# Kernel optimization log

Measured on AMD Instinct MI355X. Metric: run time of the kernel, lower is better.

The kernel has to match this reference:

```python
import jax, jax.numpy as jnp
import numpy as np

TEMPERATURE = 0.5
EPS = 1e-12  # matches torch F.normalize default eps


def _l2_normalize(x):
    norm = jnp.sqrt(jnp.sum(x * x, axis=-1, keepdims=True))
    return x / jnp.maximum(norm, EPS)


def setup_inputs() -> dict:
    key = jax.random.key(0)
    k1, k2 = jax.random.split(key)
    B, C, D = 64, 512, 256
    visual_features = jax.random.normal(k1, (B, C, D), dtype=jnp.float32)
    text_embeddings = jax.random.normal(k2, (B, C, D), dtype=jnp.float32)
    return {"visual_features": visual_features, "text_embeddings": text_embeddings}


def reference(visual_features, text_embeddings):
    v = _l2_normalize(visual_features)   # (B, C, D)
    t = _l2_normalize(text_embeddings)   # (B, C, D)
    # positive: diagonal similarity per class
    sim_pos = jnp.einsum('bcd,bcd->bc', v, t)
    positive = jnp.exp(sim_pos / TEMPERATURE)            # (B, C)
    # full BxCxC similarity matrix
    all_sim = jnp.exp(jnp.einsum('bcd,bkd->bck', v, t) / TEMPERATURE)
    negative = jnp.sum(all_sim, axis=-1) - positive      # (B, C)
    loss = -jnp.log(positive / (positive + negative))
    return jnp.mean(loss)
```

## Files before the change

### kernel.cpp

```cpp
#include <hip/hip_runtime.h>
#include <hip/hip_bf16.h>

#define BB 64
#define CC 512
#define DD 256

typedef __attribute__((ext_vector_type(8))) short bf16x8;
typedef __attribute__((ext_vector_type(4))) float f32x4;

__device__ inline short f2bf(float f) {
    union { __hip_bfloat16 h; short s; } cv;
    cv.h = __float2bfloat16(f);
    return cv.s;
}

__global__ __launch_bounds__(256, 1) void gemm_loss(const float* __restrict__ V,
                                                    const float* __restrict__ T,
                                                    float* __restrict__ partials) {
    extern __shared__ char lds[];
    char* As  = lds;
    char* Bs0 = lds + 65536;
    char* Bs1 = lds + 65536 + 32768;

    const int i0 = blockIdx.x;
    const int b  = (i0 & 7) * 8 + (i0 >> 5);
    const int rb = (i0 >> 3) & 3;

    const int tid  = threadIdx.x;
    const int lane = tid & 63;
    const int wave = tid >> 6;
    const int wr = wave >> 1;
    const int wc = wave & 1;
    const int g  = lane >> 4;
    const int ln = lane & 15;

    const float* gV = V + (size_t)b * (CC * DD) + (size_t)rb * 128 * DD;
    const float* gT = T + (size_t)b * (CC * DD);

    const int rrow = tid >> 3;
    const int ecol = (tid & 7) * 32;

    {
        float4 ar[4][8];
#pragma unroll
        for (int p = 0; p < 4; ++p) {
            const float4* src =
                reinterpret_cast<const float4*>(gV + (size_t)(p * 32 + rrow) * DD + ecol);
#pragma unroll
            for (int q = 0; q < 8; ++q) ar[p][q] = src[q];
        }
#pragma unroll
        for (int p = 0; p < 4; ++p) {
            float ss = 0.f;
#pragma unroll
            for (int q = 0; q < 8; ++q)
                ss += ar[p][q].x * ar[p][q].x + ar[p][q].y * ar[p][q].y +
                      ar[p][q].z * ar[p][q].z + ar[p][q].w * ar[p][q].w;
            ss += __shfl_xor(ss, 1);
            ss += __shfl_xor(ss, 2);
            ss += __shfl_xor(ss, 4);
            const float rinv = 1.0f / fmaxf(sqrtf(ss), 1e-12f);
            const int row = p * 32 + rrow;
            char* dstrow  = As + row * 512;
            const int sw  = (row & 7) << 4;
#pragma unroll
            for (int q2 = 0; q2 < 4; ++q2) {
                const float4 v0 = ar[p][2 * q2], v1 = ar[p][2 * q2 + 1];
                bf16x8 o;
                o[0] = f2bf(v0.x * rinv); o[1] = f2bf(v0.y * rinv);
                o[2] = f2bf(v0.z * rinv); o[3] = f2bf(v0.w * rinv);
                o[4] = f2bf(v1.x * rinv); o[5] = f2bf(v1.y * rinv);
                o[6] = f2bf(v1.z * rinv); o[7] = f2bf(v1.w * rinv);
                const int bc = ecol * 2 + q2 * 16;
                *reinterpret_cast<bf16x8*>(dstrow + (bc ^ sw)) = o;
            }
        }
    }
    {
#pragma unroll
        for (int p = 0; p < 2; ++p) {
            const float4* src =
                reinterpret_cast<const float4*>(gT + (size_t)(p * 32 + rrow) * DD + ecol);
            float4 x[8];
#pragma unroll
            for (int q = 0; q < 8; ++q) x[q] = src[q];
            float ss = 0.f;
#pragma unroll
            for (int q = 0; q < 8; ++q)
                ss += x[q].x * x[q].x + x[q].y * x[q].y + x[q].z * x[q].z + x[q].w * x[q].w;
            ss += __shfl_xor(ss, 1);
            ss += __shfl_xor(ss, 2);
            ss += __shfl_xor(ss, 4);
            const float rinv = 1.0f / fmaxf(sqrtf(ss), 1e-12f);
            const int row = p * 32 + rrow;
            char* dstrow  = Bs0 + row * 512;
            const int sw  = (row & 7) << 4;
#pragma unroll
            for (int q2 = 0; q2 < 4; ++q2) {
                const float4 v0 = x[2 * q2], v1 = x[2 * q2 + 1];
                bf16x8 o;
                o[0] = f2bf(v0.x * rinv); o[1] = f2bf(v0.y * rinv);
                o[2] = f2bf(v0.z * rinv); o[3] = f2bf(v0.w * rinv);
                o[4] = f2bf(v1.x * rinv); o[5] = f2bf(v1.y * rinv);
                o[6] = f2bf(v1.z * rinv); o[7] = f2bf(v1.w * rinv);
                const int bc = ecol * 2 + q2 * 16;
                *reinterpret_cast<bf16x8*>(dstrow + (bc ^ sw)) = o;
            }
        }
    }
    __syncthreads();

    bf16x8 a[4][8];
#pragma unroll
    for (int i = 0; i < 4; ++i) {
        const int row  = wr * 64 + i * 16 + ln;
        const char* rp = As + row * 512;
        const int sw   = (row & 7) << 4;
#pragma unroll
        for (int kk = 0; kk < 8; ++kk)
            a[i][kk] = *reinterpret_cast<const bf16x8*>(rp + ((kk * 64 + g * 16) ^ sw));
    }

    float rs[4][4];
    float dg[4][4];
#pragma unroll
    for (int i = 0; i < 4; ++i)
#pragma unroll
        for (int r = 0; r < 4; ++r) { rs[i][r] = 0.f; dg[i][r] = 0.f; }

    const f32x4 fzero = {0.f, 0.f, 0.f, 0.f};
    float4 br[2][8];
    int cur = 0;

    for (int ct = 0; ct < 8; ++ct) {
        if (ct < 7) {
            const float* gB = gT + (size_t)(ct + 1) * 64 * DD;
#pragma unroll
            for (int p = 0; p < 2; ++p) {
                const float4* src =
                    reinterpret_cast<const float4*>(gB + (size_t)(p * 32 + rrow) * DD + ecol);
#pragma unroll
                for (int q = 0; q < 8; ++q) br[p][q] = src[q];
            }
        }

        char* Bc = cur ? Bs1 : Bs0;
        f32x4 acc[4][2];
#pragma unroll
        for (int i = 0; i < 4; ++i)
#pragma unroll
            for (int j = 0; j < 2; ++j) acc[i][j] = fzero;

#pragma unroll
        for (int kk = 0; kk < 8; ++kk) {
            bf16x8 bb[2];
#pragma unroll
            for (int j = 0; j < 2; ++j) {
                const int row = wc * 32 + j * 16 + ln;
                bb[j] = *reinterpret_cast<const bf16x8*>(
                    Bc + row * 512 + (((kk * 64 + g * 16)) ^ ((row & 7) << 4)));
            }
#pragma unroll
            for (int i = 0; i < 4; ++i)
#pragma unroll
                for (int j = 0; j < 2; ++j)
                    acc[i][j] =
                        __builtin_amdgcn_mfma_f32_16x16x32_bf16(a[i][kk], bb[j], acc[i][j], 0, 0, 0);
        }

        const int gcb = ct * 64 + wc * 32;
#pragma unroll
        for (int i = 0; i < 4; ++i) {
            const int grow = rb * 128 + wr * 64 + i * 16 + g * 4;
#pragma unroll
            for (int j = 0; j < 2; ++j) {
                const int gcol = gcb + j * 16 + ln;
#pragma unroll
                for (int r = 0; r < 4; ++r) {
                    const float s2 = acc[i][j][r] * 2.0f;
                    rs[i][r] += __expf(s2);
                    if (gcol == grow + r) dg[i][r] += s2;
                }
            }
        }

        if (ct < 7) {
            char* Bn = cur ? Bs0 : Bs1;
#pragma unroll
            for (int p = 0; p < 2; ++p) {
                float ss = 0.f;
#pragma unroll
                for (int q = 0; q < 8; ++q)
                    ss += br[p][q].x * br[p][q].x + br[p][q].y * br[p][q].y +
                          br[p][q].z * br[p][q].z + br[p][q].w * br[p][q].w;
                ss += __shfl_xor(ss, 1);
                ss += __shfl_xor(ss, 2);
                ss += __shfl_xor(ss, 4);
                const float rinv = 1.0f / fmaxf(sqrtf(ss), 1e-12f);
                const int row = p * 32 + rrow;
                char* dstrow  = Bn + row * 512;
                const int sw  = (row & 7) << 4;
#pragma unroll
                for (int q2 = 0; q2 < 4; ++q2) {
                    const float4 v0 = br[p][2 * q2], v1 = br[p][2 * q2 + 1];
                    bf16x8 o;
                    o[0] = f2bf(v0.x * rinv); o[1] = f2bf(v0.y * rinv);
                    o[2] = f2bf(v0.z * rinv); o[3] = f2bf(v0.w * rinv);
                    o[4] = f2bf(v1.x * rinv); o[5] = f2bf(v1.y * rinv);
                    o[6] = f2bf(v1.z * rinv); o[7] = f2bf(v1.w * rinv);
                    const int bc = ecol * 2 + q2 * 16;
                    *reinterpret_cast<bf16x8*>(dstrow + (bc ^ sw)) = o;
                }
            }
        }
        __syncthreads();
        cur ^= 1;
    }

    float* vred = reinterpret_cast<float*>(lds);
    float* dred = vred + 256;
    float* red  = vred + 512;
#pragma unroll
    for (int i = 0; i < 4; ++i)
#pragma unroll
        for (int r = 0; r < 4; ++r) {
            float v = rs[i][r];
            float d = dg[i][r];
#pragma unroll
            for (int m = 1; m < 16; m <<= 1) {
                v += __shfl_xor(v, m);
                d += __shfl_xor(d, m);
            }
            if (ln == 0) {
                const int rl = wr * 64 + i * 16 + g * 4 + r;
                vred[rl * 2 + wc] = v;
                dred[rl * 2 + wc] = d;
            }
        }
    __syncthreads();

    float lsum = 0.f;
    if (tid < 128) {
        const float vv = vred[tid * 2] + vred[tid * 2 + 1];
        const float dd = dred[tid * 2] + dred[tid * 2 + 1];
        lsum = logf(vv) - dd;
    }
#pragma unroll
    for (int m = 1; m < 64; m <<= 1) lsum += __shfl_xor(lsum, m);
    if (lane == 0) red[wave] = lsum;
    __syncthreads();
    if (tid == 0) partials[blockIdx.x] = red[0] + red[1] + red[2] + red[3];
}

__global__ __launch_bounds__(256) void final_reduce(const float* __restrict__ partials,
                                                    float* __restrict__ out) {
    const int t = threadIdx.x;
    float v = partials[t];
#pragma unroll
    for (int m = 1; m < 64; m <<= 1) v += __shfl_xor(v, m);
    __shared__ float red[4];
    if ((t & 63) == 0) red[t >> 6] = v;
    __syncthreads();
    if (t == 0) out[0] = (red[0] + red[1] + red[2] + red[3]) * (1.0f / 32768.0f);
}

extern "C" void kernel_launch(void* const* d_in, const int* in_sizes, int n_in,
                              void* d_out, int out_size, void* d_ws, size_t ws_size,
                              hipStream_t stream) {
    const float* vis = (const float*)d_in[0];
    const float* txt = (const float*)d_in[1];

    float* partials = (float*)d_ws;
    float* out      = (float*)d_out;

    hipFuncSetAttribute((const void*)gemm_loss, hipFuncAttributeMaxDynamicSharedMemorySize,
                        131072);

    gemm_loss<<<256, 256, 131072, stream>>>(vis, txt, partials);
    final_reduce<<<1, 256, 0, stream>>>(partials, out);
}
```

Measured before the change: 43.95 us.

## Halve row tile to 64, launch 512 blocks with two-buffer LDS reuse

Each block now handles 64 visual rows instead of 128, so the grid doubles to 512 blocks and LDS per block drops from 128KB to 64KB, which allows two blocks per CU. The A tile is read into registers and its LDS buffer is then reused as the second B ping-pong buffer. Waves now split the column tile, one 16-column strip each, rather than a 2x2 arrangement. The aim is better occupancy and a more even spread of work across the CUs. The cost is that each text tile is loaded and normalized twice as often in total.

```diff
diff --git a/kernel.cpp b/kernel.cpp
--- a/kernel.cpp
+++ b/kernel.cpp
@@ -7,6 +7,8 @@
 
 typedef __attribute__((ext_vector_type(8))) short bf16x8;
 typedef __attribute__((ext_vector_type(4))) float f32x4;
+
+#define SW(row) (((row) & 7) << 4)
 
 __device__ inline short f2bf(float f) {
     union { __hip_bfloat16 h; short s; } cv;
@@ -14,112 +16,85 @@
     return cv.s;
 }
 
-__global__ __launch_bounds__(256, 1) void gemm_loss(const float* __restrict__ V,
+__device__ inline void reduce_write(char* dst_base, int row, int ecolB, const float4* x) {
+    float ss = 0.f;
+#pragma unroll
+    for (int q = 0; q < 8; ++q)
+        ss += x[q].x * x[q].x + x[q].y * x[q].y + x[q].z * x[q].z + x[q].w * x[q].w;
+    ss += __shfl_xor(ss, 1);
+    ss += __shfl_xor(ss, 2);
+    ss += __shfl_xor(ss, 4);
+    const float rinv = 1.0f / fmaxf(sqrtf(ss), 1e-12f);
+    char* dstrow = dst_base + row * 512;
+    const int sw = SW(row);
+#pragma unroll
+    for (int q2 = 0; q2 < 4; ++q2) {
+        const float4 v0 = x[2 * q2], v1 = x[2 * q2 + 1];
+        bf16x8 o;
+        o[0] = f2bf(v0.x * rinv); o[1] = f2bf(v0.y * rinv);
+        o[2] = f2bf(v0.z * rinv); o[3] = f2bf(v0.w * rinv);
+        o[4] = f2bf(v1.x * rinv); o[5] = f2bf(v1.y * rinv);
+        o[6] = f2bf(v1.z * rinv); o[7] = f2bf(v1.w * rinv);
+        *reinterpret_cast<bf16x8*>(dstrow + ((ecolB + q2 * 16) ^ sw)) = o;
+    }
+}
+
+__global__ __launch_bounds__(256, 2) void gemm_loss(const float* __restrict__ V,
                                                     const float* __restrict__ T,
                                                     float* __restrict__ partials) {
     extern __shared__ char lds[];
-    char* As  = lds;
-    char* Bs0 = lds + 65536;
-    char* Bs1 = lds + 65536 + 32768;
+    char* BufA = lds;
+    char* BufB = lds + 32768;
 
     const int i0 = blockIdx.x;
-    const int b  = (i0 & 7) * 8 + (i0 >> 5);
-    const int rb = (i0 >> 3) & 3;
+    const int b  = (i0 & 7) * 8 + ((i0 >> 3) & 7);
+    const int rb = i0 >> 6;
 
     const int tid  = threadIdx.x;
     const int lane = tid & 63;
     const int wave = tid >> 6;
-    const int wr = wave >> 1;
-    const int wc = wave & 1;
-    const int g  = lane >> 4;
-    const int ln = lane & 15;
-
-    const float* gV = V + (size_t)b * (CC * DD) + (size_t)rb * 128 * DD;
+    const int g    = lane >> 4;
+    const int ln   = lane & 15;
+    const int rrow = tid >> 3;
+    const int ecolB = (tid & 7) * 64;
+
+    const float* gV = V + (size_t)b * (CC * DD) + (size_t)rb * 64 * DD;
     const float* gT = T + (size_t)b * (CC * DD);
 
-    const int rrow = tid >> 3;
-    const int ecol = (tid & 7) * 32;
-
     {
-        float4 ar[4][8];
-#pragma unroll
-        for (int p = 0; p < 4; ++p) {
-            const float4* src =
-                reinterpret_cast<const float4*>(gV + (size_t)(p * 32 + rrow) * DD + ecol);
-#pragma unroll
-            for (int q = 0; q < 8; ++q) ar[p][q] = src[q];
-        }
-#pragma unroll
-        for (int p = 0; p < 4; ++p) {
-            float ss = 0.f;
-#pragma unroll
-            for (int q = 0; q < 8; ++q)
-                ss += ar[p][q].x * ar[p][q].x + ar[p][q].y * ar[p][q].y +
-                      ar[p][q].z * ar[p][q].z + ar[p][q].w * ar[p][q].w;
-            ss += __shfl_xor(ss, 1);
-            ss += __shfl_xor(ss, 2);
-            ss += __shfl_xor(ss, 4);
-            const float rinv = 1.0f / fmaxf(sqrtf(ss), 1e-12f);
-            const int row = p * 32 + rrow;
-            char* dstrow  = As + row * 512;
-            const int sw  = (row & 7) << 4;
-#pragma unroll
-            for (int q2 = 0; q2 < 4; ++q2) {
-                const float4 v0 = ar[p][2 * q2], v1 = ar[p][2 * q2 + 1];
-                bf16x8 o;
-                o[0] = f2bf(v0.x * rinv); o[1] = f2bf(v0.y * rinv);
-                o[2] = f2bf(v0.z * rinv); o[3] = f2bf(v0.w * rinv);
-                o[4] = f2bf(v1.x * rinv); o[5] = f2bf(v1.y * rinv);
-                o[6] = f2bf(v1.z * rinv); o[7] = f2bf(v1.w * rinv);
-                const int bc = ecol * 2 + q2 * 16;
-                *reinterpret_cast<bf16x8*>(dstrow + (bc ^ sw)) = o;
-            }
-        }
-    }
-    {
+        float4 xs[4][8];
 #pragma unroll
         for (int p = 0; p < 2; ++p) {
             const float4* src =
-                reinterpret_cast<const float4*>(gT + (size_t)(p * 32 + rrow) * DD + ecol);
-            float4 x[8];
-#pragma unroll
-            for (int q = 0; q < 8; ++q) x[q] = src[q];
-            float ss = 0.f;
-#pragma unroll
-            for (int q = 0; q < 8; ++q)
-                ss += x[q].x * x[q].x + x[q].y * x[q].y + x[q].z * x[q].z + x[q].w * x[q].w;
-            ss += __shfl_xor(ss, 1);
-            ss += __shfl_xor(ss, 2);
-            ss += __shfl_xor(ss, 4);
-            const float rinv = 1.0f / fmaxf(sqrtf(ss), 1e-12f);
-            const int row = p * 32 + rrow;
-            char* dstrow  = Bs0 + row * 512;
-            const int sw  = (row & 7) << 4;
-#pragma unroll
-            for (int q2 = 0; q2 < 4; ++q2) {
-                const float4 v0 = x[2 * q2], v1 = x[2 * q2 + 1];
-                bf16x8 o;
-                o[0] = f2bf(v0.x * rinv); o[1] = f2bf(v0.y * rinv);
-                o[2] = f2bf(v0.z * rinv); o[3] = f2bf(v0.w * rinv);
-                o[4] = f2bf(v1.x * rinv); o[5] = f2bf(v1.y * rinv);
-                o[6] = f2bf(v1.z * rinv); o[7] = f2bf(v1.w * rinv);
-                const int bc = ecol * 2 + q2 * 16;
-                *reinterpret_cast<bf16x8*>(dstrow + (bc ^ sw)) = o;
-            }
-        }
+                reinterpret_cast<const float4*>(gV + (size_t)(p * 32 + rrow) * DD + (tid & 7) * 32);
+#pragma unroll
+            for (int q = 0; q < 8; ++q) xs[p][q] = src[q];
+        }
+#pragma unroll
+        for (int p = 0; p < 2; ++p) {
+            const float4* src =
+                reinterpret_cast<const float4*>(gT + (size_t)(p * 32 + rrow) * DD + (tid & 7) * 32);
+#pragma unroll
+            for (int q = 0; q < 8; ++q) xs[2 + p][q] = src[q];
+        }
+#pragma unroll
+        for (int p = 0; p < 2; ++p) reduce_write(BufA, p * 32 + rrow, ecolB, xs[p]);
+#pragma unroll
+        for (int p = 0; p < 2; ++p) reduce_write(BufB, p * 32 + rrow, ecolB, xs[2 + p]);
     }
     __syncthreads();
 
     bf16x8 a[4][8];
 #pragma unroll
     for (int i = 0; i < 4; ++i) {
-        const int row  = wr * 64 + i * 16 + ln;
-        const char* rp = As + row * 512;
-        const int sw   = (row & 7) << 4;
+        const int row  = i * 16 + ln;
+        const char* rp = BufA + row * 512;
+        const int sw   = SW(row);
 #pragma unroll
         for (int kk = 0; kk < 8; ++kk)
             a[i][kk] = *reinterpret_cast<const bf16x8*>(rp + ((kk * 64 + g * 16) ^ sw));
     }
+    __syncthreads();
 
     float rs[4][4];
     float dg[4][4];
@@ -128,98 +103,61 @@
 #pragma unroll
         for (int r = 0; r < 4; ++r) { rs[i][r] = 0.f; dg[i][r] = 0.f; }
 
-    const f32x4 fzero = {0.f, 0.f, 0.f, 0.f};
-    float4 br[2][8];
-    int cur = 0;
+    float4 x[8];
 
     for (int ct = 0; ct < 8; ++ct) {
         if (ct < 7) {
-            const float* gB = gT + (size_t)(ct + 1) * 64 * DD;
-#pragma unroll
-            for (int p = 0; p < 2; ++p) {
-                const float4* src =
-                    reinterpret_cast<const float4*>(gB + (size_t)(p * 32 + rrow) * DD + ecol);
-#pragma unroll
-                for (int q = 0; q < 8; ++q) br[p][q] = src[q];
-            }
-        }
-
-        char* Bc = cur ? Bs1 : Bs0;
-        f32x4 acc[4][2];
-#pragma unroll
-        for (int i = 0; i < 4; ++i)
-#pragma unroll
-            for (int j = 0; j < 2; ++j) acc[i][j] = fzero;
-
-#pragma unroll
-        for (int kk = 0; kk < 8; ++kk) {
-            bf16x8 bb[2];
-#pragma unroll
-            for (int j = 0; j < 2; ++j) {
-                const int row = wc * 32 + j * 16 + ln;
-                bb[j] = *reinterpret_cast<const bf16x8*>(
-                    Bc + row * 512 + (((kk * 64 + g * 16)) ^ ((row & 7) << 4)));
-            }
-#pragma unroll
-            for (int i = 0; i < 4; ++i)
-#pragma unroll
-                for (int j = 0; j < 2; ++j)
-                    acc[i][j] =
-                        __builtin_amdgcn_mfma_f32_16x16x32_bf16(a[i][kk], bb[j], acc[i][j], 0, 0, 0);
-        }
-
-        const int gcb = ct * 64 + wc * 32;
+            const float4* src = reinterpret_cast<const float4*>(
+                gT + (size_t)((ct + 1) * 64 + rrow) * DD + (tid & 7) * 32);
+#pragma unroll
+            for (int q = 0; q < 8; ++q) x[q] = src[q];
+        }
+
+        const char* Bc = (ct & 1) ? BufA : BufB;
+        f32x4 acc[4];
+#pragma unroll
+        for (int i = 0; i < 4; ++i) acc[i] = (f32x4){0.f, 0.f, 0.f, 0.f};
+        {
+            const int row  = wave * 16 + ln;
+            const char* rp = Bc + row * 512;
+            const int sw   = SW(row);
+#pragma unroll
+            for (int kk = 0; kk < 8; ++kk) {
+                const bf16x8 bb =
+                    *reinterpret_cast<const bf16x8*>(rp + ((kk * 64 + g * 16) ^ sw));
+#pragma unroll
+                for (int i = 0; i < 4; ++i)
+                    acc[i] = __builtin_amdgcn_mfma_f32_16x16x32_bf16(a[i][kk], bb, acc[i], 0, 0, 0);
+            }
+        }
+
+        char* Bn = (ct & 1) ? BufB : BufA;
+        if (ct < 7) {
+            reduce_write(Bn, rrow, ecolB, x);
+            const float4* src = reinterpret_cast<const float4*>(
+                gT + (size_t)((ct + 1) * 64 + 32 + rrow) * DD + (tid & 7) * 32);
+#pragma unroll
+            for (int q = 0; q < 8; ++q) x[q] = src[q];
+        }
+
+        const int gcol = ct * 64 + wave * 16 + ln;
 #pragma unroll
         for (int i = 0; i < 4; ++i) {
-            const int grow = rb * 128 + wr * 64 + i * 16 + g * 4;
-#pragma unroll
-            for (int j = 0; j < 2; ++j) {
-                const int gcol = gcb + j * 16 + ln;
-#pragma unroll
-                for (int r = 0; r < 4; ++r) {
-                    const float s2 = acc[i][j][r] * 2.0f;
-                    rs[i][r] += __expf(s2);
-                    if (gcol == grow + r) dg[i][r] += s2;
-                }
-            }
-        }
-
-        if (ct < 7) {
-            char* Bn = cur ? Bs0 : Bs1;
-#pragma unroll
-            for (int p = 0; p < 2; ++p) {
-                float ss = 0.f;
-#pragma unroll
-                for (int q = 0; q < 8; ++q)
-                    ss += br[p][q].x * br[p][q].x + br[p][q].y * br[p][q].y +
-                          br[p][q].z * br[p][q].z + br[p][q].w * br[p][q].w;
-                ss += __shfl_xor(ss, 1);
-                ss += __shfl_xor(ss, 2);
-                ss += __shfl_xor(ss, 4);
-                const float rinv = 1.0f / fmaxf(sqrtf(ss), 1e-12f);
-                const int row = p * 32 + rrow;
-                char* dstrow  = Bn + row * 512;
-                const int sw  = (row & 7) << 4;
-#pragma unroll
-                for (int q2 = 0; q2 < 4; ++q2) {
-                    const float4 v0 = br[p][2 * q2], v1 = br[p][2 * q2 + 1];
-                    bf16x8 o;
-                    o[0] = f2bf(v0.x * rinv); o[1] = f2bf(v0.y * rinv);
-                    o[2] = f2bf(v0.z * rinv); o[3] = f2bf(v0.w * rinv);
-                    o[4] = f2bf(v1.x * rinv); o[5] = f2bf(v1.y * rinv);
-                    o[6] = f2bf(v1.z * rinv); o[7] = f2bf(v1.w * rinv);
-                    const int bc = ecol * 2 + q2 * 16;
-                    *reinterpret_cast<bf16x8*>(dstrow + (bc ^ sw)) = o;
-                }
-            }
-        }
+            const int grow = rb * 64 + i * 16 + g * 4;
+#pragma unroll
+            for (int r = 0; r < 4; ++r) {
+                const float s2 = acc[i][r] * 2.0f;
+                rs[i][r] += __expf(s2);
+                if (gcol == grow + r) dg[i][r] += s2;
+            }
+        }
+
+        if (ct < 7) reduce_write(Bn, 32 + rrow, ecolB, x);
         __syncthreads();
-        cur ^= 1;
-    }
-
-    float* vred = reinterpret_cast<float*>(lds);
+    }
+
+    float* vred = reinterpret_cast<float*>(BufB);
     float* dred = vred + 256;
-    float* red  = vred + 512;
 #pragma unroll
     for (int i = 0; i < 4; ++i)
 #pragma unroll
@@ -232,30 +170,27 @@
                 d += __shfl_xor(d, m);
             }
             if (ln == 0) {
-                const int rl = wr * 64 + i * 16 + g * 4 + r;
-                vred[rl * 2 + wc] = v;
-                dred[rl * 2 + wc] = d;
-            }
-        }
-    __syncthreads();
-
-    float lsum = 0.f;
-    if (tid < 128) {
-        const float vv = vred[tid * 2] + vred[tid * 2 + 1];
-        const float dd = dred[tid * 2] + dred[tid * 2 + 1];
-        lsum = logf(vv) - dd;
-    }
-#pragma unroll
-    for (int m = 1; m < 64; m <<= 1) lsum += __shfl_xor(lsum, m);
-    if (lane == 0) red[wave] = lsum;
-    __syncthreads();
-    if (tid == 0) partials[blockIdx.x] = red[0] + red[1] + red[2] + red[3];
+                const int rl = i * 16 + g * 4 + r;
+                vred[rl * 4 + wave] = v;
+                dred[rl * 4 + wave] = d;
+            }
+        }
+    __syncthreads();
+
+    if (wave == 0) {
+        const float vv = vred[lane * 4] + vred[lane * 4 + 1] + vred[lane * 4 + 2] + vred[lane * 4 + 3];
+        const float dd = dred[lane * 4] + dred[lane * 4 + 1] + dred[lane * 4 + 2] + dred[lane * 4 + 3];
+        float lsum = logf(vv) - dd;
+#pragma unroll
+        for (int m = 1; m < 64; m <<= 1) lsum += __shfl_xor(lsum, m);
+        if (lane == 0) partials[i0] = lsum;
+    }
 }
 
 __global__ __launch_bounds__(256) void final_reduce(const float* __restrict__ partials,
                                                     float* __restrict__ out) {
     const int t = threadIdx.x;
-    float v = partials[t];
+    float v = partials[t] + partials[t + 256];
 #pragma unroll
     for (int m = 1; m < 64; m <<= 1) v += __shfl_xor(v, m);
     __shared__ float red[4];
@@ -274,8 +209,8 @@
     float* out      = (float*)d_out;
 
     hipFuncSetAttribute((const void*)gemm_loss, hipFuncAttributeMaxDynamicSharedMemorySize,
-                        131072);
-
-    gemm_loss<<<256, 256, 131072, stream>>>(vis, txt, partials);
+                        65536);
+
+    gemm_loss<<<512, 256, 65536, stream>>>(vis, txt, partials);
     final_reduce<<<1, 256, 0, stream>>>(partials, out);
 }
```

Result: slower. 56.84 us (+29.3%).
